# Kernel tuning notes

Hardware: AMD Instinct MI355X
Metric: run time of the kernel (lower is better)

Reference implementation:

```python
import jax, jax.numpy as jnp
import numpy as np

LN_EPS = 1e-6


def setup_inputs() -> dict:
    key = jax.random.key(0)
    ks = jax.random.split(key, 8)
    B, T, V, r, c, D = 1, 2048, 50257, 16, 16, 1024
    rc = r * c
    return {
        "input_ids": jax.random.randint(ks[0], (B, T), 0, V),
        "token_to_mu_w": jax.random.normal(ks[1], (rc, V), jnp.float32) * 0.02,  # nn.Linear(V, rc).weight
        "pos_embedding": jax.random.normal(ks[2], (1, T, r, c), jnp.float32) * 0.02,
        "w1": jax.random.normal(ks[3], (D, rc), jnp.float32) * 0.05,  # Linear(rc, D).weight
        "b1": jnp.zeros((D,), jnp.float32),
        "ln_w": jnp.ones((D,), jnp.float32),
        "ln_b": jnp.zeros((D,), jnp.float32),
        "w2": jax.random.normal(ks[4], (V, D), jnp.float32) * 0.02,  # Linear(D, V).weight
        "b2": jnp.zeros((V,), jnp.float32),
    }


def reference(input_ids, token_to_mu_w, pos_embedding, w1, b1, ln_w, ln_b, w2, b2):
    B, T = input_ids.shape
    r, c = pos_embedding.shape[2], pos_embedding.shape[3]
    # one_hot(input_ids) @ W^T is exactly a row-gather of W^T (single nonzero per row)
    MU = jnp.take(token_to_mu_w.T, input_ids, axis=0)          # [B, T, rc]
    MU = MU.reshape(B, T, r, c) + pos_embedding[:, :T]         # [B, T, r, c]
    # n_layers = 0: no transformer blocks; dropout is identity in eval
    x = MU.reshape(B, T, r * c)
    h = jax.nn.gelu(jnp.einsum('btk,dk->btd', x, w1) + b1, approximate=False)
    mean = jnp.mean(h, axis=-1, keepdims=True)
    var = jnp.mean(jnp.square(h - mean), axis=-1, keepdims=True)
    h = (h - mean) * jax.lax.rsqrt(var + LN_EPS) * ln_w + ln_b
    logits = jnp.einsum('btd,vd->btv', h, w2) + b2             # [B, T, V]
    return logits, MU
```

## Files before the change

kernel.cpp:

```cpp
#include <hip/hip_runtime.h>
#include <hip/hip_bf16.h>
#include <math.h>

#define T_LEN 2048
#define RC 256
#define DIM 1024
#define VOCAB 50257

using short8 = __attribute__((ext_vector_type(8))) short;
using f32x4  = __attribute__((ext_vector_type(4))) float;

__device__ __forceinline__ unsigned short f2bf(float f) {
    unsigned int u = __float_as_uint(f);
    u += 0x7fffu + ((u >> 16) & 1u);
    return (unsigned short)(u >> 16);
}

__device__ __forceinline__ void async_load16(void* lds, const void* g) {
    __builtin_amdgcn_global_load_lds(
        (const __attribute__((address_space(1))) void*)g,
        (__attribute__((address_space(3))) void*)lds,
        16, 0, 0);
}

__global__ __launch_bounds__(256) void mu_kernel(
    const int* __restrict__ ids, const float* __restrict__ tokw,
    const float* __restrict__ pos, float* __restrict__ mu) {
    int t = blockIdx.x, k = threadIdx.x;
    int id = ids[t];
    float v = tokw[(size_t)k * VOCAB + id] + pos[t * RC + k];
    mu[t * RC + k] = v;
}

__global__ __launch_bounds__(256) void gemm1_gelu_kernel(
    const float* __restrict__ mu, const float* __restrict__ w1,
    const float* __restrict__ b1, float* __restrict__ hpre) {
    __shared__ float xs[16][RC];
    const int tg = blockIdx.x, ng = blockIdx.y, tid = threadIdx.x;
    const int t0 = tg * 16;
    {
        const float4* src = (const float4*)(mu + (size_t)t0 * RC);
        float4* dst = (float4*)&xs[0][0];
        #pragma unroll
        for (int i = 0; i < 4; ++i) dst[tid + 256 * i] = src[tid + 256 * i];
    }
    __syncthreads();
    const int d = ng * 256 + tid;
    float acc[16];
    const float bias = b1[d];
    #pragma unroll
    for (int t = 0; t < 16; ++t) acc[t] = bias;
    const float4* w1r = (const float4*)(w1 + (size_t)d * RC);
    for (int k4 = 0; k4 < RC / 4; ++k4) {
        const float4 w = w1r[k4];
        #pragma unroll
        for (int t = 0; t < 16; ++t) {
            const float4 xv = *(const float4*)&xs[t][k4 * 4];
            acc[t] += w.x * xv.x + w.y * xv.y + w.z * xv.z + w.w * xv.w;
        }
    }
    #pragma unroll
    for (int t = 0; t < 16; ++t) {
        float x = acc[t];
        float g = 0.5f * x * (1.0f + erff(x * 0.70710678118654752f));
        hpre[(size_t)(t0 + t) * DIM + d] = g;
    }
}

__global__ __launch_bounds__(256) void ln_kernel(
    const float* __restrict__ hpre, const float* __restrict__ lnw,
    const float* __restrict__ lnb, unsigned short* __restrict__ h) {
    const int t = blockIdx.x, tid = threadIdx.x;
    const float4 v = ((const float4*)(hpre + (size_t)t * DIM))[tid];
    float s  = v.x + v.y + v.z + v.w;
    float ss = v.x * v.x + v.y * v.y + v.z * v.z + v.w * v.w;
    #pragma unroll
    for (int off = 32; off > 0; off >>= 1) {
        s  += __shfl_down(s, off, 64);
        ss += __shfl_down(ss, off, 64);
    }
    __shared__ float red[8];
    const int wid = tid >> 6, lane = tid & 63;
    if (lane == 0) { red[wid] = s; red[4 + wid] = ss; }
    __syncthreads();
    const float S  = red[0] + red[1] + red[2] + red[3];
    const float SS = red[4] + red[5] + red[6] + red[7];
    const float mean = S * (1.0f / DIM);
    const float var  = SS * (1.0f / DIM) - mean * mean;
    const float inv  = 1.0f / sqrtf(var + 1e-6f);
    const float4 wv = ((const float4*)lnw)[tid];
    const float4 bv = ((const float4*)lnb)[tid];
    ushort4 o;
    o.x = f2bf((v.x - mean) * inv * wv.x + bv.x);
    o.y = f2bf((v.y - mean) * inv * wv.y + bv.y);
    o.z = f2bf((v.z - mean) * inv * wv.z + bv.z);
    o.w = f2bf((v.w - mean) * inv * wv.w + bv.w);
    ((ushort4*)h)[(size_t)t * (DIM / 4) + tid] = o;
}

__global__ __launch_bounds__(256) void cvt_kernel(
    const float* __restrict__ src, unsigned short* __restrict__ dst, int n4) {
    int i = blockIdx.x * 256 + threadIdx.x;
    const int stride = gridDim.x * 256;
    for (; i < n4; i += stride) {
        const float4 v = ((const float4*)src)[i];
        ushort4 o;
        o.x = f2bf(v.x); o.y = f2bf(v.y); o.z = f2bf(v.z); o.w = f2bf(v.w);
        ((ushort4*)dst)[i] = o;
    }
}

__global__ __launch_bounds__(256) void gemm2_kernel(
    const unsigned short* __restrict__ A, const unsigned short* __restrict__ B,
    const float* __restrict__ b2, float* __restrict__ out) {
    __shared__ unsigned short As[128 * 64];
    __shared__ unsigned short Bs[128 * 64];

    const int tid  = threadIdx.x;
    const int bid  = blockIdx.x;
    const int m0   = (bid & 15) << 7;
    const int n0   = (bid >> 4) << 7;
    const int wid  = tid >> 6;
    const int lane = tid & 63;
    const int wm   = wid >> 1, wn = wid & 1;
    const int lr   = lane & 15;
    const int lk   = lane >> 4;

    const f32x4 zero = {0.f, 0.f, 0.f, 0.f};
    f32x4 acc[4][4];
    #pragma unroll
    for (int m = 0; m < 4; ++m)
        #pragma unroll
        for (int n = 0; n < 4; ++n) acc[m][n] = zero;

    for (int kt = 0; kt < DIM / 64; ++kt) {
        #pragma unroll
        for (int it = 0; it < 4; ++it) {
            const int g   = it * 256 + tid;
            const int row = g >> 3, c8 = g & 7;
            async_load16(As + g * 8,
                         A + (size_t)(m0 + row) * DIM + kt * 64 + c8 * 8);
            int bn = n0 + row; if (bn > VOCAB - 1) bn = VOCAB - 1;
            async_load16(Bs + g * 8,
                         B + (size_t)bn * DIM + kt * 64 + c8 * 8);
        }
        __syncthreads();
        #pragma unroll
        for (int kk = 0; kk < 2; ++kk) {
            short8 af[4], bfr[4];
            #pragma unroll
            for (int m = 0; m < 4; ++m)
                af[m] = *(const short8*)&As[(wm * 64 + m * 16 + lr) * 64 + kk * 32 + lk * 8];
            #pragma unroll
            for (int n = 0; n < 4; ++n)
                bfr[n] = *(const short8*)&Bs[(wn * 64 + n * 16 + lr) * 64 + kk * 32 + lk * 8];
            #pragma unroll
            for (int m = 0; m < 4; ++m)
                #pragma unroll
                for (int n = 0; n < 4; ++n)
                    acc[m][n] = __builtin_amdgcn_mfma_f32_16x16x32_bf16(
                        af[m], bfr[n], acc[m][n], 0, 0, 0);
        }
        __syncthreads();
    }

    #pragma unroll
    for (int m = 0; m < 4; ++m) {
        const int row = m0 + wm * 64 + m * 16 + lk * 4;
        #pragma unroll
        for (int n = 0; n < 4; ++n) {
            const int col = n0 + wn * 64 + n * 16 + lr;
            if (col < VOCAB) {
                const float bias = b2[col];
                #pragma unroll
                for (int j = 0; j < 4; ++j)
                    out[(size_t)(row + j) * VOCAB + col] = acc[m][n][j] + bias;
            }
        }
    }
}

extern "C" void kernel_launch(void* const* d_in, const int* in_sizes, int n_in,
                              void* d_out, int out_size, void* d_ws, size_t ws_size,
                              hipStream_t stream) {
    (void)in_sizes; (void)n_in; (void)out_size; (void)ws_size;
    const int*   ids  = (const int*)d_in[0];
    const float* tokw = (const float*)d_in[1];
    const float* pos  = (const float*)d_in[2];
    const float* w1   = (const float*)d_in[3];
    const float* b1   = (const float*)d_in[4];
    const float* lnw  = (const float*)d_in[5];
    const float* lnb  = (const float*)d_in[6];
    const float* w2   = (const float*)d_in[7];
    const float* b2   = (const float*)d_in[8];

    float* logits = (float*)d_out;
    float* mu_out = logits + (size_t)T_LEN * VOCAB;

    unsigned short* w2b = (unsigned short*)d_ws;
    unsigned short* hb  = (unsigned short*)((char*)d_ws + (size_t)VOCAB * DIM * 2);
    float* hpre = logits;

    mu_kernel<<<dim3(T_LEN), dim3(256), 0, stream>>>(ids, tokw, pos, mu_out);
    gemm1_gelu_kernel<<<dim3(T_LEN / 16, DIM / 256), dim3(256), 0, stream>>>(
        mu_out, w1, b1, hpre);
    ln_kernel<<<dim3(T_LEN), dim3(256), 0, stream>>>(hpre, lnw, lnb, hb);
    cvt_kernel<<<dim3(2048), dim3(256), 0, stream>>>(
        w2, w2b, (int)((size_t)VOCAB * DIM / 4));
    const int ntiles_n = (VOCAB + 127) / 128;
    gemm2_kernel<<<dim3(16 * ntiles_n), dim3(256), 0, stream>>>(hb, w2b, b2, logits);
}
```

Baseline: 569.6 us.

## Rewrite vocab GEMM with 256x256 tiles, 4-stage async LDS pipeline, swizzle

The logits GEMM moves from 128x128 tiles with a single LDS buffer and full syncs to 256x256 tiles on 512 threads. It uses a 4-slot ring of K=32 LDS stages with three tiles prefetched, explicit vmcnt waits, split barriers and raised priority around the MFMA blocks. An XOR swizzle on the LDS layout avoids bank conflicts, and a block-id remap groups tiles by XCD for L2 reuse. The aim is to hide global load latency behind MFMA work and raise arithmetic intensity per tile. In exchange it adds higher register pressure and fragile hand-counted waitcnt logic.

```diff
diff --git a/kernel.cpp b/kernel.cpp
--- a/kernel.cpp
+++ b/kernel.cpp
@@ -6,9 +6,14 @@
 #define RC 256
 #define DIM 1024
 #define VOCAB 50257
+#define NT 32
+#define SLOT 8192
 
 using short8 = __attribute__((ext_vector_type(8))) short;
 using f32x4  = __attribute__((ext_vector_type(4))) float;
+
+#define VMCNT(n) asm volatile("s_waitcnt vmcnt(" #n ")" ::: "memory")
+#define SCHED_FENCE() __builtin_amdgcn_sched_barrier(0)
 
 __device__ __forceinline__ unsigned short f2bf(float f) {
     unsigned int u = __float_as_uint(f);
@@ -110,66 +115,114 @@
     }
 }
 
-__global__ __launch_bounds__(256) void gemm2_kernel(
+__device__ __forceinline__ void stage_tile_part(
+    const unsigned short* __restrict__ A, const unsigned short* __restrict__ B,
+    unsigned short* As_s, unsigned short* Bs_s,
+    int m0, int n0, int kt, int it, int tid, int lk_src) {
+    const int row = it * 128 + (tid >> 2);
+    async_load16(As_s + (size_t)(it * 512 + tid) * 8,
+                 A + (size_t)(m0 + row) * DIM + kt * 32 + lk_src * 8);
+    int bn = n0 + row; if (bn > VOCAB - 1) bn = VOCAB - 1;
+    async_load16(Bs_s + (size_t)(it * 512 + tid) * 8,
+                 B + (size_t)bn * DIM + kt * 32 + lk_src * 8);
+}
+
+__global__ __launch_bounds__(512, 2) void gemm2_kernel(
     const unsigned short* __restrict__ A, const unsigned short* __restrict__ B,
     const float* __restrict__ b2, float* __restrict__ out) {
-    __shared__ unsigned short As[128 * 64];
-    __shared__ unsigned short Bs[128 * 64];
+    __shared__ unsigned short As[4 * SLOT];
+    __shared__ unsigned short Bs[4 * SLOT];
 
     const int tid  = threadIdx.x;
-    const int bid  = blockIdx.x;
-    const int m0   = (bid & 15) << 7;
-    const int n0   = (bid >> 4) << 7;
-    const int wid  = tid >> 6;
+    const int cpx  = gridDim.x >> 3;
+    const int wgid = (blockIdx.x & 7) * cpx + (blockIdx.x >> 3);
+    const int m0   = (wgid & 7) << 8;
+    const int n0   = (wgid >> 3) << 8;
+
     const int lane = tid & 63;
-    const int wm   = wid >> 1, wn = wid & 1;
     const int lr   = lane & 15;
     const int lk   = lane >> 4;
-
-    const f32x4 zero = {0.f, 0.f, 0.f, 0.f};
-    f32x4 acc[4][4];
-    #pragma unroll
-    for (int m = 0; m < 4; ++m)
-        #pragma unroll
-        for (int n = 0; n < 4; ++n) acc[m][n] = zero;
-
-    for (int kt = 0; kt < DIM / 64; ++kt) {
-        #pragma unroll
-        for (int it = 0; it < 4; ++it) {
-            const int g   = it * 256 + tid;
-            const int row = g >> 3, c8 = g & 7;
-            async_load16(As + g * 8,
-                         A + (size_t)(m0 + row) * DIM + kt * 64 + c8 * 8);
-            int bn = n0 + row; if (bn > VOCAB - 1) bn = VOCAB - 1;
-            async_load16(Bs + g * 8,
-                         B + (size_t)bn * DIM + kt * 64 + c8 * 8);
-        }
-        __syncthreads();
-        #pragma unroll
-        for (int kk = 0; kk < 2; ++kk) {
-            short8 af[4], bfr[4];
-            #pragma unroll
-            for (int m = 0; m < 4; ++m)
-                af[m] = *(const short8*)&As[(wm * 64 + m * 16 + lr) * 64 + kk * 32 + lk * 8];
+    const int wid  = tid >> 6;
+    const int wr   = wid >> 2;
+    const int wc   = wid & 3;
+    const int xr      = (lk ^ ((lr >> 1) & 3)) * 8;
+    const int arow0   = wr * 128 + lr;
+    const int brow0   = wc * 64 + lr;
+    const int lk_src  = (tid & 3) ^ ((tid >> 3) & 3);
+
+    f32x4 acc[8][4];
+    #pragma unroll
+    for (int m = 0; m < 8; ++m)
+        #pragma unroll
+        for (int n = 0; n < 4; ++n) acc[m][n] = {0.f, 0.f, 0.f, 0.f};
+
+    #pragma unroll
+    for (int tt = 0; tt < 3; ++tt) {
+        stage_tile_part(A, B, As + tt * SLOT, Bs + tt * SLOT, m0, n0, tt, 0, tid, lk_src);
+        stage_tile_part(A, B, As + tt * SLOT, Bs + tt * SLOT, m0, n0, tt, 1, tid, lk_src);
+        SCHED_FENCE();
+    }
+    VMCNT(8);
+    __builtin_amdgcn_s_barrier();
+
+    #pragma unroll 1
+    for (int t = 0; t < NT; ++t) {
+        const unsigned short* As_t = As + (t & 3) * SLOT;
+        const unsigned short* Bs_t = Bs + (t & 3) * SLOT;
+        unsigned short* As_s = As + ((t + 3) & 3) * SLOT;
+        unsigned short* Bs_s = Bs + ((t + 3) & 3) * SLOT;
+        const bool do_stage = (t + 3 < NT);
+        short8 af[4], bf[4];
+
+        #pragma unroll
+        for (int n = 0; n < 4; ++n)
+            bf[n] = *(const short8*)(Bs_t + (brow0 + n * 16) * 32 + xr);
+        #pragma unroll
+        for (int m = 0; m < 4; ++m)
+            af[m] = *(const short8*)(As_t + (arow0 + m * 16) * 32 + xr);
+        if (do_stage)
+            stage_tile_part(A, B, As_s, Bs_s, m0, n0, t + 3, 0, tid, lk_src);
+        SCHED_FENCE();
+        __builtin_amdgcn_s_barrier();
+        __builtin_amdgcn_s_setprio(1);
+        #pragma unroll
+        for (int m = 0; m < 4; ++m)
             #pragma unroll
             for (int n = 0; n < 4; ++n)
-                bfr[n] = *(const short8*)&Bs[(wn * 64 + n * 16 + lr) * 64 + kk * 32 + lk * 8];
+                acc[m][n] = __builtin_amdgcn_mfma_f32_16x16x32_bf16(
+                    af[m], bf[n], acc[m][n], 0, 0, 0);
+        __builtin_amdgcn_s_setprio(0);
+        SCHED_FENCE();
+        __builtin_amdgcn_s_barrier();
+
+        #pragma unroll
+        for (int m = 0; m < 4; ++m)
+            af[m] = *(const short8*)(As_t + (arow0 + (m + 4) * 16) * 32 + xr);
+        if (do_stage)
+            stage_tile_part(A, B, As_s, Bs_s, m0, n0, t + 3, 1, tid, lk_src);
+        SCHED_FENCE();
+        if (t < NT - 3)       { VMCNT(8); }
+        else if (t == NT - 3) { VMCNT(4); }
+        else                  { VMCNT(0); }
+        __builtin_amdgcn_s_barrier();
+        __builtin_amdgcn_s_setprio(1);
+        #pragma unroll
+        for (int m = 0; m < 4; ++m)
             #pragma unroll
-            for (int m = 0; m < 4; ++m)
-                #pragma unroll
-                for (int n = 0; n < 4; ++n)
-                    acc[m][n] = __builtin_amdgcn_mfma_f32_16x16x32_bf16(
-                        af[m], bfr[n], acc[m][n], 0, 0, 0);
-        }
-        __syncthreads();
-    }
-
-    #pragma unroll
-    for (int m = 0; m < 4; ++m) {
-        const int row = m0 + wm * 64 + m * 16 + lk * 4;
+            for (int n = 0; n < 4; ++n)
+                acc[m + 4][n] = __builtin_amdgcn_mfma_f32_16x16x32_bf16(
+                    af[m], bf[n], acc[m + 4][n], 0, 0, 0);
+        __builtin_amdgcn_s_setprio(0);
+        SCHED_FENCE();
+        __builtin_amdgcn_s_barrier();
+    }
+
+    #pragma unroll
+    for (int m = 0; m < 8; ++m) {
+        const int row = m0 + wr * 128 + m * 16 + lk * 4;
         #pragma unroll
         for (int n = 0; n < 4; ++n) {
-            const int col = n0 + wn * 64 + n * 16 + lr;
+            const int col = n0 + wc * 64 + n * 16 + lr;
             if (col < VOCAB) {
                 const float bias = b2[col];
                 #pragma unroll
@@ -207,6 +260,6 @@
     ln_kernel<<<dim3(T_LEN), dim3(256), 0, stream>>>(hpre, lnw, lnb, hb);
     cvt_kernel<<<dim3(2048), dim3(256), 0, stream>>>(
         w2, w2b, (int)((size_t)VOCAB * DIM / 4));
-    const int ntiles_n = (VOCAB + 127) / 128;
-    gemm2_kernel<<<dim3(16 * ntiles_n), dim3(256), 0, stream>>>(hb, w2b, b2, logits);
-}
+    const int ntiles_n = (VOCAB + 255) / 256;
+    gemm2_kernel<<<dim3(8 * ntiles_n), dim3(512), 0, stream>>>(hb, w2b, b2, logits);
+}
```

New measurement: 491.6 us. 1.16x faster.

## Triple-buffer gemm2 LDS tiles with async prefetch, swizzle, and XCD remap

Applied to the files above, without the earlier changes.

Rewrites the logits GEMM main loop to use a three-slot LDS ring with K=32 tiles. Loads for tile t+2 are issued while tile t is computed, and completion is tracked with explicit vmcnt waits and raw barriers. It also XOR-swizzles the LDS layout to reduce bank conflicts, remaps block IDs across the 8 XCDs for L2 locality, raises MFMA priority, and sets launch bounds for 3 blocks per CU. The aim is to hide global-load latency behind MFMA work, at the cost of more fragile manual synchronization.

```diff
diff --git a/kernel.cpp b/kernel.cpp
--- a/kernel.cpp
+++ b/kernel.cpp
@@ -6,9 +6,14 @@
 #define RC 256
 #define DIM 1024
 #define VOCAB 50257
+#define NT 32
+#define SLOT 4096
 
 using short8 = __attribute__((ext_vector_type(8))) short;
 using f32x4  = __attribute__((ext_vector_type(4))) float;
+
+#define VMCNT(n) asm volatile("s_waitcnt vmcnt(" #n ")" ::: "memory")
+#define SCHED_FENCE() __builtin_amdgcn_sched_barrier(0)
 
 __device__ __forceinline__ unsigned short f2bf(float f) {
     unsigned int u = __float_as_uint(f);
@@ -110,71 +115,110 @@
     }
 }
 
-__global__ __launch_bounds__(256) void gemm2_kernel(
+__device__ __forceinline__ void stage_tile(
+    const unsigned short* __restrict__ A, const unsigned short* __restrict__ B,
+    unsigned short* As_s, unsigned short* Bs_s,
+    int m0, int n0, int kt, int tid, int lk_src) {
+    #pragma unroll
+    for (int p = 0; p < 2; ++p) {
+        const int g = p * 256 + tid;
+        const int row = g >> 2;
+        async_load16(As_s + (size_t)g * 8,
+                     A + (size_t)(m0 + row) * DIM + kt * 32 + lk_src * 8);
+    }
+    #pragma unroll
+    for (int p = 0; p < 2; ++p) {
+        const int g = p * 256 + tid;
+        const int row = g >> 2;
+        int bn = n0 + row; if (bn > VOCAB - 1) bn = VOCAB - 1;
+        async_load16(Bs_s + (size_t)g * 8,
+                     B + (size_t)bn * DIM + kt * 32 + lk_src * 8);
+    }
+}
+
+__global__ __launch_bounds__(256, 3) void gemm2_kernel(
     const unsigned short* __restrict__ A, const unsigned short* __restrict__ B,
     const float* __restrict__ b2, float* __restrict__ out) {
-    __shared__ unsigned short As[128 * 64];
-    __shared__ unsigned short Bs[128 * 64];
+    __shared__ unsigned short As[3 * SLOT];
+    __shared__ unsigned short Bs[3 * SLOT];
 
     const int tid  = threadIdx.x;
-    const int bid  = blockIdx.x;
-    const int m0   = (bid & 15) << 7;
-    const int n0   = (bid >> 4) << 7;
-    const int wid  = tid >> 6;
+    const int cpx  = gridDim.x >> 3;
+    const int wgid = (blockIdx.x & 7) * cpx + (blockIdx.x >> 3);
+    const int m0   = (wgid & 15) << 7;
+    const int n0   = (wgid >> 4) << 7;
+
     const int lane = tid & 63;
-    const int wm   = wid >> 1, wn = wid & 1;
     const int lr   = lane & 15;
     const int lk   = lane >> 4;
-
-    const f32x4 zero = {0.f, 0.f, 0.f, 0.f};
+    const int wid  = tid >> 6;
+    const int wr   = wid >> 1;
+    const int wc   = wid & 1;
+    const int xr     = (lk ^ ((lr >> 1) & 3)) * 8;
+    const int arow0  = wr * 64 + lr;
+    const int brow0  = wc * 64 + lr;
+    const int lk_src = (tid & 3) ^ ((tid >> 3) & 3);
+
     f32x4 acc[4][4];
     #pragma unroll
     for (int m = 0; m < 4; ++m)
         #pragma unroll
-        for (int n = 0; n < 4; ++n) acc[m][n] = zero;
-
-    for (int kt = 0; kt < DIM / 64; ++kt) {
-        #pragma unroll
-        for (int it = 0; it < 4; ++it) {
-            const int g   = it * 256 + tid;
-            const int row = g >> 3, c8 = g & 7;
-            async_load16(As + g * 8,
-                         A + (size_t)(m0 + row) * DIM + kt * 64 + c8 * 8);
-            int bn = n0 + row; if (bn > VOCAB - 1) bn = VOCAB - 1;
-            async_load16(Bs + g * 8,
-                         B + (size_t)bn * DIM + kt * 64 + c8 * 8);
-        }
-        __syncthreads();
-        #pragma unroll
-        for (int kk = 0; kk < 2; ++kk) {
-            short8 af[4], bfr[4];
-            #pragma unroll
-            for (int m = 0; m < 4; ++m)
-                af[m] = *(const short8*)&As[(wm * 64 + m * 16 + lr) * 64 + kk * 32 + lk * 8];
+        for (int n = 0; n < 4; ++n) acc[m][n] = {0.f, 0.f, 0.f, 0.f};
+
+    stage_tile(A, B, As, Bs, m0, n0, 0, tid, lk_src);
+    SCHED_FENCE();
+    stage_tile(A, B, As + SLOT, Bs + SLOT, m0, n0, 1, tid, lk_src);
+    SCHED_FENCE();
+    VMCNT(4);
+    __builtin_amdgcn_s_barrier();
+
+    int cur = 0, st2 = 2;
+    #pragma unroll 1
+    for (int t = 0; t < NT; ++t) {
+        const unsigned short* As_t = As + cur * SLOT;
+        const unsigned short* Bs_t = Bs + cur * SLOT;
+        short8 af[4], bf[4];
+        #pragma unroll
+        for (int m = 0; m < 4; ++m)
+            af[m] = *(const short8*)(As_t + (arow0 + m * 16) * 32 + xr);
+        #pragma unroll
+        for (int n = 0; n < 4; ++n)
+            bf[n] = *(const short8*)(Bs_t + (brow0 + n * 16) * 32 + xr);
+        if (t + 2 < NT)
+            stage_tile(A, B, As + st2 * SLOT, Bs + st2 * SLOT, m0, n0, t + 2, tid, lk_src);
+        SCHED_FENCE();
+        if (t < NT - 2) { VMCNT(4); } else { VMCNT(0); }
+        __builtin_amdgcn_s_barrier();
+        __builtin_amdgcn_s_setprio(1);
+        #pragma unroll
+        for (int m = 0; m < 4; ++m)
             #pragma unroll
             for (int n = 0; n < 4; ++n)
-                bfr[n] = *(const short8*)&Bs[(wn * 64 + n * 16 + lr) * 64 + kk * 32 + lk * 8];
-            #pragma unroll
-            for (int m = 0; m < 4; ++m)
-                #pragma unroll
-                for (int n = 0; n < 4; ++n)
-                    acc[m][n] = __builtin_amdgcn_mfma_f32_16x16x32_bf16(
-                        af[m], bfr[n], acc[m][n], 0, 0, 0);
-        }
-        __syncthreads();
-    }
-
+                acc[m][n] = __builtin_amdgcn_mfma_f32_16x16x32_bf16(
+                    af[m], bf[n], acc[m][n], 0, 0, 0);
+        __builtin_amdgcn_s_setprio(0);
+        SCHED_FENCE();
+        __builtin_amdgcn_s_barrier();
+        if (++cur == 3) cur = 0;
+        if (++st2 == 3) st2 = 0;
+    }
+
+    float bias[4]; int col[4]; bool ok[4];
+    #pragma unroll
+    for (int n = 0; n < 4; ++n) {
+        col[n] = n0 + wc * 64 + n * 16 + lr;
+        ok[n]  = col[n] < VOCAB;
+        bias[n] = ok[n] ? b2[col[n]] : 0.f;
+    }
     #pragma unroll
     for (int m = 0; m < 4; ++m) {
-        const int row = m0 + wm * 64 + m * 16 + lk * 4;
+        const int row = m0 + wr * 64 + m * 16 + lk * 4;
         #pragma unroll
         for (int n = 0; n < 4; ++n) {
-            const int col = n0 + wn * 64 + n * 16 + lr;
-            if (col < VOCAB) {
-                const float bias = b2[col];
+            if (ok[n]) {
                 #pragma unroll
                 for (int j = 0; j < 4; ++j)
-                    out[(size_t)(row + j) * VOCAB + col] = acc[m][n][j] + bias;
+                    out[(size_t)(row + j) * VOCAB + col[n]] = acc[m][n][j] + bias[n];
             }
         }
     }
```

Result: faster. 476.6 us (-16.3%).
